# Optimization experiments

Measured on AMD Instinct MI355X. Metric: run time of the kernel, lower is better.

Reference implementation:

```python
import jax, jax.numpy as jnp
import numpy as np

T, D, H = 65536, 256, 256


def setup_inputs() -> dict:
    key = jax.random.key(0)
    ks = jax.random.split(key, 6)
    lim = 1.0 / np.sqrt(H)  # equinox GRUCell init: U(-1/sqrt(hidden), 1/sqrt(hidden))
    x = jax.random.normal(ks[0], (T, D), dtype=jnp.float32)
    state = jnp.zeros((H,), dtype=jnp.float32)
    start = jax.random.randint(ks[1], (T,), 0, 2).astype(jnp.int32)  # episode-start mask
    next_done = jnp.zeros((T,), dtype=jnp.int32)  # unused by forward, kept for signature fidelity
    W_ih = jax.random.uniform(ks[2], (3 * H, D), minval=-lim, maxval=lim, dtype=jnp.float32)
    W_hh = jax.random.uniform(ks[3], (3 * H, H), minval=-lim, maxval=lim, dtype=jnp.float32)
    bias = jax.random.uniform(ks[4], (3 * H,), minval=-lim, maxval=lim, dtype=jnp.float32)
    bias_n = jax.random.uniform(ks[5], (H,), minval=-lim, maxval=lim, dtype=jnp.float32)
    return {"x": x, "state": state, "start": start, "next_done": next_done,
            "W_ih": W_ih, "W_hh": W_hh, "bias": bias, "bias_n": bias_n}


def reference(x, state, start, next_done, W_ih, W_hh, bias, bias_n):
    # Input-dependent gate pre-activations for all timesteps in one big GEMM: [T, 3H]
    igates_all = x @ W_ih.T + bias
    start_f = start.astype(x.dtype)

    def step(h, inp):
        ig, s = inp
        h = h * (1.0 - s)  # reset hidden at episode start (state * logical_not(start))
        hg = W_hh @ h  # [3H]
        r = jax.nn.sigmoid(ig[:H] + hg[:H])
        z = jax.nn.sigmoid(ig[H:2 * H] + hg[H:2 * H])
        n = jnp.tanh(ig[2 * H:] + r * (hg[2 * H:] + bias_n))
        new_h = n + z * (h - n)  # equinox GRUCell output
        return new_h, new_h

    final_state, y = jax.lax.scan(step, state, (igates_all, start_f))
    return y, final_state
```

## Files before the change

kernel.cpp:

```cpp
#include <hip/hip_runtime.h>
#include <hip/hip_bf16.h>
#include <stdint.h>

#define TT   65536
#define NCH  16
#define CNOM 16
#define NBLK 256
#define ROWB 1664

typedef __bf16 bf16x8 __attribute__((ext_vector_type(8)));
typedef float  f32x4  __attribute__((ext_vector_type(4)));
typedef int    i32x4  __attribute__((ext_vector_type(4)));

__device__ __bf16 g_wih[768 * 256];
__device__ __bf16 g_whh[768 * 256];
__device__ __align__(64) unsigned char g_ig[(size_t)TT * ROWB];

__device__ __forceinline__ void gl_lds16(const void* g, void* l) {
  __builtin_amdgcn_global_load_lds(
      (const __attribute__((address_space(1))) void*)(unsigned long long)(uintptr_t)g,
      (__attribute__((address_space(3))) void*)(unsigned int)(uintptr_t)l,
      16, 0, 0);
}

__device__ __forceinline__ float bfbits(uint32_t u) {
  float f; __builtin_memcpy(&f, &u, 4); return f;
}

__device__ __forceinline__ void mfma_bv0(f32x4& acc, bf16x8 a, i32x4 b) {
  asm("v_mfma_f32_16x16x32_bf16 %0, %1, %2, 0" : "=&v"(acc) : "v"(a), "v"(b));
}
__device__ __forceinline__ void mfma_ba0(f32x4& acc, bf16x8 a, i32x4 b) {
  asm("v_mfma_f32_16x16x32_bf16 %0, %1, %2, 0" : "=&v"(acc) : "v"(a), "a"(b));
}
__device__ __forceinline__ void mfma_bv(f32x4& acc, bf16x8 a, i32x4 b) {
  asm("v_mfma_f32_16x16x32_bf16 %0, %1, %2, %0" : "+v"(acc) : "v"(a), "v"(b));
}
__device__ __forceinline__ void mfma_ba(f32x4& acc, bf16x8 a, i32x4 b) {
  asm("v_mfma_f32_16x16x32_bf16 %0, %1, %2, %0" : "+v"(acc) : "v"(a), "a"(b));
}

__global__ void prep_w(const float* __restrict__ wih, const float* __restrict__ whh) {
  const int n = 768 * 256;
  for (int i = blockIdx.x * blockDim.x + threadIdx.x; i < n; i += gridDim.x * blockDim.x) {
    g_wih[i] = (__bf16)wih[i];
    g_whh[i] = (__bf16)whh[i];
  }
}

__global__ __launch_bounds__(256) void gemm_ig(const float* __restrict__ x,
                                               const float* __restrict__ bias) {
  __shared__ __align__(16) __bf16 a_s[128 * 64];
  __shared__ __align__(16) __bf16 b_s[128 * 64];
  const int tid = threadIdx.x;
  const int w = tid >> 6, lane = tid & 63, l15 = lane & 15, q = lane >> 4;
  const int mt = blockIdx.x / 6, ntb = blockIdx.x - mt * 6;
  const int m0 = mt * 128, n0 = ntb * 128;
  const int wm = w >> 1, wn = w & 1;

  f32x4 acc[4][4];
#pragma unroll
  for (int a = 0; a < 4; ++a)
#pragma unroll
    for (int b = 0; b < 4; ++b) acc[a][b] = (f32x4){0.f, 0.f, 0.f, 0.f};

  for (int kc = 0; kc < 4; ++kc) {
#pragma unroll
    for (int i = 0; i < 4; ++i) {
      int pslot = i * 256 + tid;
      int row = pslot >> 3, c = pslot & 7;
      int cs = c ^ (row & 7);
      const float* xs = x + (size_t)(m0 + row) * 256 + kc * 64 + cs * 8;
      float4 f0 = *(const float4*)xs;
      float4 f1 = *(const float4*)(xs + 4);
      bf16x8 v;
      v[0] = (__bf16)f0.x; v[1] = (__bf16)f0.y; v[2] = (__bf16)f0.z; v[3] = (__bf16)f0.w;
      v[4] = (__bf16)f1.x; v[5] = (__bf16)f1.y; v[6] = (__bf16)f1.z; v[7] = (__bf16)f1.w;
      *(bf16x8*)((char*)a_s + pslot * 16) = v;
      gl_lds16((const char*)g_wih + ((size_t)(n0 + row) * 256 + kc * 64) * 2 + cs * 16,
               (char*)b_s + (i * 256 + (tid & ~63)) * 16);
    }
    __syncthreads();
#pragma unroll
    for (int ks = 0; ks < 2; ++ks) {
      bf16x8 af[4], bfr[4];
#pragma unroll
      for (int tm = 0; tm < 4; ++tm) {
        int row = wm * 64 + tm * 16 + l15;
        int cb = (ks * 4 + q) ^ (row & 7);
        af[tm] = *(const bf16x8*)((const char*)a_s + row * 128 + cb * 16);
      }
#pragma unroll
      for (int tn = 0; tn < 4; ++tn) {
        int row = wn * 64 + tn * 16 + l15;
        int cb = (ks * 4 + q) ^ (row & 7);
        bfr[tn] = *(const bf16x8*)((const char*)b_s + row * 128 + cb * 16);
      }
#pragma unroll
      for (int tm = 0; tm < 4; ++tm)
#pragma unroll
        for (int tn = 0; tn < 4; ++tn)
          acc[tm][tn] = __builtin_amdgcn_mfma_f32_16x16x32_bf16(af[tm], bfr[tn], acc[tm][tn], 0, 0, 0);
    }
    __syncthreads();
  }
  float bv[4];
#pragma unroll
  for (int tn = 0; tn < 4; ++tn) bv[tn] = bias[n0 + wn * 64 + tn * 16 + l15];
#pragma unroll
  for (int tm = 0; tm < 4; ++tm) {
#pragma unroll
    for (int tp = 0; tp < 2; ++tp) {
#pragma unroll
      for (int r = 0; r < 4; ++r) {
        int t = m0 + wm * 64 + tm * 16 + q * 4 + r;
        __bf16 lo = (__bf16)(acc[tm][tp * 2][r] + bv[tp * 2]);
        __bf16 hi = (__bf16)(acc[tm][tp * 2 + 1][r] + bv[tp * 2 + 1]);
        unsigned short ulo, uhi;
        __builtin_memcpy(&ulo, &lo, 2); __builtin_memcpy(&uhi, &hi, 2);
        uint32_t u = (uint32_t)ulo | ((uint32_t)uhi << 16);
        *(uint32_t*)(g_ig + (size_t)t * ROWB + ntb * 256 + (wn * 2 + tp) * 64 + l15 * 4) = u;
      }
    }
  }
}

__global__ __launch_bounds__(512)
__attribute__((amdgpu_waves_per_eu(2, 2)))
void gru_scan(const float* __restrict__ state, const int* __restrict__ start,
              const float* __restrict__ bias_n, float* __restrict__ out) {
  __shared__ __align__(16) __bf16 h_s[2][16][264];
  __shared__ __align__(16) unsigned char whh_lds[8 * 16 * 1024];
  __shared__ int flg_s[16 * 132];
  __shared__ int s_arr[17];

  const int tid = threadIdx.x;
  const int w = tid >> 6, lane = tid & 63, l15 = lane & 15, q = lane >> 4;
  const int jrow0 = w * 32 + l15;

  if (tid < 17) {
    int t = (blockIdx.x * NCH + tid) * CNOM;
    if (t > 0) { while (t < TT && start[t] == 0) t++; }
    s_arr[tid] = t;
  }
  for (int i = tid; i < 16 * 264; i += 512) (&h_s[0][0][0])[i] = (__bf16)0.f;
  __syncthreads();

  int sa[4], len[4];
#pragma unroll
  for (int r = 0; r < 4; ++r) {
    sa[r] = s_arr[q * 4 + r];
    len[r] = s_arr[q * 4 + r + 1] - sa[r];
  }
  int ML = 0;
  for (int m = 0; m < 16; ++m) { int L = s_arr[m + 1] - s_arr[m]; ML = L > ML ? L : ML; }
  ML = __builtin_amdgcn_readfirstlane(ML);

  for (int idx = tid; idx < 2048; idx += 512) {
    int m = idx >> 7, kk = idx & 127;
    int t = s_arr[m] + kk;
    flg_s[m * 132 + kk] = (t < TT) ? start[t] : 0;
  }

  char* lp = (char*)whh_lds + w * 16384 + lane * 16;
#pragma unroll
  for (int p = 0; p < 2; ++p)
#pragma unroll
    for (int ks = 0; ks < 8; ++ks) {
      i32x4 t = *(const i32x4*)&g_whh[(size_t)(w * 32 + p * 16 + l15) * 256 + q * 8 + ks * 32];
      *(i32x4*)(lp + (p * 8 + ks) * 1024) = t;
    }
  i32x4 whh_z[2][8], whh_n[2][8];
#pragma unroll
  for (int p = 0; p < 2; ++p)
#pragma unroll
    for (int ks = 0; ks < 8; ++ks) {
      whh_z[p][ks] = *(const i32x4*)&g_whh[(size_t)(1 * 256 + w * 32 + p * 16 + l15) * 256 + q * 8 + ks * 32];
      whh_n[p][ks] = *(const i32x4*)&g_whh[(size_t)(2 * 256 + w * 32 + p * 16 + l15) * 256 + q * 8 + ks * 32];
    }
#pragma unroll
  for (int p = 0; p < 2; ++p)
#pragma unroll
    for (int ks = 0; ks < 8; ++ks) {
      asm volatile("" : "+a"(whh_z[p][ks]));
      asm volatile("" : "+a"(whh_n[p][ks]));
    }

  const float bn2[2] = { bias_n[jrow0], bias_n[jrow0 + 16] };

  const int start0 = start[0];
  if (blockIdx.x == 0 && tid < 256) h_s[0][0][tid] = start0 ? (__bf16)0.f : (__bf16)state[tid];

  float hreg[2][4];
#pragma unroll
  for (int p = 0; p < 2; ++p)
#pragma unroll
    for (int r = 0; r < 4; ++r) hreg[p][r] = 0.f;
  if (blockIdx.x == 0 && q == 0 && !start0) {
    hreg[0][0] = state[jrow0];
    hreg[1][0] = state[jrow0 + 16];
  }

  const int cw = (w >> 2) * 256 + ((w & 3) * 16 + l15) * 4;
  const uint32_t offlim = (uint32_t)(TT - 1) * ROWB + (uint32_t)cw;
  uint32_t off[4];
  float* op[4];
#pragma unroll
  for (int r = 0; r < 4; ++r) {
    off[r] = (uint32_t)sa[r] * ROWB + (uint32_t)cw;
    op[r] = out + (size_t)sa[r] * 256 + jrow0;
  }

  const unsigned char* gig = g_ig;
  uint32_t igA[12], igB[12];
#pragma unroll
  for (int r = 0; r < 4; ++r) {
    igA[r * 3 + 0] = *(const uint32_t*)(gig + off[r]);
    igA[r * 3 + 1] = *(const uint32_t*)(gig + off[r] + 512);
    igA[r * 3 + 2] = *(const uint32_t*)(gig + off[r] + 1024);
    uint32_t nx = off[r] + ROWB; off[r] = nx > offlim ? offlim : nx;
  }
  __syncthreads();

  auto step = [&](int k, uint32_t (&cur)[12], uint32_t (&nxt)[12]) {
#pragma unroll
    for (int r = 0; r < 4; ++r) {
      nxt[r * 3 + 0] = *(const uint32_t*)(gig + off[r]);
      nxt[r * 3 + 1] = *(const uint32_t*)(gig + off[r] + 512);
      nxt[r * 3 + 2] = *(const uint32_t*)(gig + off[r] + 1024);
      uint32_t nx = off[r] + ROWB; off[r] = nx > offlim ? offlim : nx;
    }
    int fnext[4];
    if (k + 1 < 128) {
#pragma unroll
      for (int r = 0; r < 4; ++r) fnext[r] = flg_s[(q * 4 + r) * 132 + k + 1];
    } else {
#pragma unroll
      for (int r = 0; r < 4; ++r) {
        int t = sa[r] + k + 1; t = t > TT - 1 ? TT - 1 : t;
        fnext[r] = start[t];
      }
    }

    const __bf16* hb = &h_s[k & 1][0][0] + l15 * 264 + q * 8;
#pragma unroll
    for (int p = 0; p < 2; ++p) {
      f32x4 a0, a1, a2;
      {
        bf16x8 hf = *(const bf16x8*)(hb);
        i32x4 b0 = *(const i32x4*)(lp + (p * 8) * 1024);
        mfma_bv0(a0, hf, b0);
        mfma_ba0(a1, hf, whh_z[p][0]);
        mfma_ba0(a2, hf, whh_n[p][0]);
      }
#pragma unroll
      for (int ks = 1; ks < 8; ++ks) {
        bf16x8 hf = *(const bf16x8*)(hb + ks * 32);
        i32x4 b0 = *(const i32x4*)(lp + (p * 8 + ks) * 1024);
        mfma_bv(a0, hf, b0);
        mfma_ba(a1, hf, whh_z[p][ks]);
        mfma_ba(a2, hf, whh_n[p][ks]);
      }
      asm volatile("s_nop 7\n\ts_nop 7" : "+v"(a0), "+v"(a1), "+v"(a2));
#pragma unroll
      for (int r = 0; r < 4; ++r) {
        uint32_t vr = cur[r * 3 + 0];
        uint32_t vz = cur[r * 3 + 1];
        uint32_t vn = cur[r * 3 + 2];
        float igr = bfbits(p ? (vr & 0xffff0000u) : (vr << 16));
        float igz = bfbits(p ? (vz & 0xffff0000u) : (vz << 16));
        float ign = bfbits(p ? (vn & 0xffff0000u) : (vn << 16));
        float rp_ = a0[r] + igr;
        float zp_ = a1[r] + igz;
        float hv  = a2[r] + bn2[p];
        float rg = 1.f / (1.f + __expf(-rp_));
        float zg = 1.f / (1.f + __expf(-zp_));
        float np = ign + rg * hv;
        np = fminf(fmaxf(np, -30.f), 30.f);
        float e2 = __expf(2.f * np);
        float ng = (e2 - 1.f) / (e2 + 1.f);
        float hn = ng + zg * (hreg[p][r] - ng);
        if (k < len[r]) op[r][p * 16] = hn;
        hreg[p][r] = fnext[r] ? 0.f : hn;
      }
    }
    __bf16* hw = &h_s[(k + 1) & 1][0][0];
#pragma unroll
    for (int p = 0; p < 2; ++p)
#pragma unroll
      for (int r = 0; r < 4; ++r)
        hw[(q * 4 + r) * 264 + jrow0 + p * 16] = (__bf16)hreg[p][r];
#pragma unroll
    for (int r = 0; r < 4; ++r) op[r] += 256;
    asm volatile("s_waitcnt lgkmcnt(0)" ::: "memory");
    __builtin_amdgcn_s_barrier();
  };

  for (int k = 0; k < ML; ) {
    step(k, igA, igB); ++k;
    if (k < ML) { step(k, igB, igA); ++k; }
  }
}

__global__ void fin_copy(float* __restrict__ out) {
  int i = threadIdx.x;
  out[(size_t)TT * 256 + i] = out[((size_t)TT - 1) * 256 + i];
}

extern "C" void kernel_launch(void* const* d_in, const int* in_sizes, int n_in,
                              void* d_out, int out_size, void* d_ws, size_t ws_size,
                              hipStream_t stream) {
  const float* x      = (const float*)d_in[0];
  const float* state  = (const float*)d_in[1];
  const int*   start  = (const int*)d_in[2];
  const float* wih    = (const float*)d_in[4];
  const float* whh    = (const float*)d_in[5];
  const float* bias   = (const float*)d_in[6];
  const float* bias_n = (const float*)d_in[7];
  float* out = (float*)d_out;

  prep_w<<<256, 256, 0, stream>>>(wih, whh);
  gemm_ig<<<3072, 256, 0, stream>>>(x, bias);
  gru_scan<<<NBLK, 512, 0, stream>>>(state, start, bias_n, out);
  fin_copy<<<1, 256, 0, stream>>>(out);
}
```

Baseline: 304.0 us.

## Keep x tile resident in LDS and stream W_ih with double buffering

The input-gate GEMM now has each 512-thread block own a 128-row strip of x. That strip is converted to bf16 once and kept in LDS across all six 128-column output tiles. W_ih is read as fp32 and converted inline, with double-buffered prefetch of the next chunk, so the separate bf16 copy of W_ih in prep_w goes away. This removes the sixfold re-read and re-conversion of x across blocks. In exchange the grid is smaller (512 blocks), LDS use is larger (96KB), and W_ih is converted redundantly in every block.

```diff
diff --git a/kernel.cpp b/kernel.cpp
--- a/kernel.cpp
+++ b/kernel.cpp
@@ -12,17 +12,9 @@
 typedef float  f32x4  __attribute__((ext_vector_type(4)));
 typedef int    i32x4  __attribute__((ext_vector_type(4)));
 
-__device__ __bf16 g_wih[768 * 256];
 __device__ __bf16 g_whh[768 * 256];
 __device__ __align__(64) unsigned char g_ig[(size_t)TT * ROWB];
 
-__device__ __forceinline__ void gl_lds16(const void* g, void* l) {
-  __builtin_amdgcn_global_load_lds(
-      (const __attribute__((address_space(1))) void*)(unsigned long long)(uintptr_t)g,
-      (__attribute__((address_space(3))) void*)(unsigned int)(uintptr_t)l,
-      16, 0, 0);
-}
-
 __device__ __forceinline__ float bfbits(uint32_t u) {
   float f; __builtin_memcpy(&f, &u, 4); return f;
 }
@@ -40,87 +32,126 @@
   asm("v_mfma_f32_16x16x32_bf16 %0, %1, %2, %0" : "+v"(acc) : "v"(a), "a"(b));
 }
 
-__global__ void prep_w(const float* __restrict__ wih, const float* __restrict__ whh) {
+__device__ __forceinline__ bf16x8 cvt8(float4 f0, float4 f1) {
+  bf16x8 v;
+  v[0] = (__bf16)f0.x; v[1] = (__bf16)f0.y; v[2] = (__bf16)f0.z; v[3] = (__bf16)f0.w;
+  v[4] = (__bf16)f1.x; v[5] = (__bf16)f1.y; v[6] = (__bf16)f1.z; v[7] = (__bf16)f1.w;
+  return v;
+}
+
+__global__ void prep_w(const float* __restrict__ whh) {
   const int n = 768 * 256;
-  for (int i = blockIdx.x * blockDim.x + threadIdx.x; i < n; i += gridDim.x * blockDim.x) {
-    g_wih[i] = (__bf16)wih[i];
+  for (int i = blockIdx.x * blockDim.x + threadIdx.x; i < n; i += gridDim.x * blockDim.x)
     g_whh[i] = (__bf16)whh[i];
-  }
-}
-
-__global__ __launch_bounds__(256) void gemm_ig(const float* __restrict__ x,
+}
+
+__global__ __launch_bounds__(512) void gemm_ig(const float* __restrict__ x,
+                                               const float* __restrict__ wih,
                                                const float* __restrict__ bias) {
-  __shared__ __align__(16) __bf16 a_s[128 * 64];
-  __shared__ __align__(16) __bf16 b_s[128 * 64];
+  __shared__ __align__(16) __bf16 a_s[4][128 * 64];
+  __shared__ __align__(16) __bf16 b_s[2][128 * 64];
   const int tid = threadIdx.x;
-  const int w = tid >> 6, lane = tid & 63, l15 = lane & 15, q = lane >> 4;
-  const int mt = blockIdx.x / 6, ntb = blockIdx.x - mt * 6;
-  const int m0 = mt * 128, n0 = ntb * 128;
-  const int wm = w >> 1, wn = w & 1;
-
-  f32x4 acc[4][4];
-#pragma unroll
-  for (int a = 0; a < 4; ++a)
-#pragma unroll
-    for (int b = 0; b < 4; ++b) acc[a][b] = (f32x4){0.f, 0.f, 0.f, 0.f};
-
-  for (int kc = 0; kc < 4; ++kc) {
-#pragma unroll
-    for (int i = 0; i < 4; ++i) {
-      int pslot = i * 256 + tid;
-      int row = pslot >> 3, c = pslot & 7;
-      int cs = c ^ (row & 7);
+  const int lane = tid & 63, l15 = lane & 15, q = lane >> 4;
+  const int w = tid >> 6;
+  const int wm = w >> 2, wn = w & 3;
+  const int m0 = blockIdx.x * 128;
+
+  float bvA[6], bvB[6];
+#pragma unroll
+  for (int nb = 0; nb < 6; ++nb) {
+    bvA[nb] = bias[nb * 128 + wn * 32 + l15];
+    bvB[nb] = bias[nb * 128 + wn * 32 + 16 + l15];
+  }
+
+#pragma unroll
+  for (int kc = 0; kc < 4; ++kc)
+#pragma unroll
+    for (int i = 0; i < 2; ++i) {
+      int pslot = i * 512 + tid;
+      int row = pslot >> 3, c = pslot & 7, cs = c ^ (row & 7);
       const float* xs = x + (size_t)(m0 + row) * 256 + kc * 64 + cs * 8;
       float4 f0 = *(const float4*)xs;
       float4 f1 = *(const float4*)(xs + 4);
-      bf16x8 v;
-      v[0] = (__bf16)f0.x; v[1] = (__bf16)f0.y; v[2] = (__bf16)f0.z; v[3] = (__bf16)f0.w;
-      v[4] = (__bf16)f1.x; v[5] = (__bf16)f1.y; v[6] = (__bf16)f1.z; v[7] = (__bf16)f1.w;
-      *(bf16x8*)((char*)a_s + pslot * 16) = v;
-      gl_lds16((const char*)g_wih + ((size_t)(n0 + row) * 256 + kc * 64) * 2 + cs * 16,
-               (char*)b_s + (i * 256 + (tid & ~63)) * 16);
-    }
-    __syncthreads();
-#pragma unroll
-    for (int ks = 0; ks < 2; ++ks) {
-      bf16x8 af[4], bfr[4];
-#pragma unroll
-      for (int tm = 0; tm < 4; ++tm) {
-        int row = wm * 64 + tm * 16 + l15;
-        int cb = (ks * 4 + q) ^ (row & 7);
-        af[tm] = *(const bf16x8*)((const char*)a_s + row * 128 + cb * 16);
-      }
-#pragma unroll
-      for (int tn = 0; tn < 4; ++tn) {
-        int row = wn * 64 + tn * 16 + l15;
-        int cb = (ks * 4 + q) ^ (row & 7);
-        bfr[tn] = *(const bf16x8*)((const char*)b_s + row * 128 + cb * 16);
-      }
-#pragma unroll
-      for (int tm = 0; tm < 4; ++tm)
-#pragma unroll
-        for (int tn = 0; tn < 4; ++tn)
-          acc[tm][tn] = __builtin_amdgcn_mfma_f32_16x16x32_bf16(af[tm], bfr[tn], acc[tm][tn], 0, 0, 0);
-    }
-    __syncthreads();
-  }
-  float bv[4];
-#pragma unroll
-  for (int tn = 0; tn < 4; ++tn) bv[tn] = bias[n0 + wn * 64 + tn * 16 + l15];
-#pragma unroll
-  for (int tm = 0; tm < 4; ++tm) {
-#pragma unroll
-    for (int tp = 0; tp < 2; ++tp) {
-#pragma unroll
-      for (int r = 0; r < 4; ++r) {
-        int t = m0 + wm * 64 + tm * 16 + q * 4 + r;
-        __bf16 lo = (__bf16)(acc[tm][tp * 2][r] + bv[tp * 2]);
-        __bf16 hi = (__bf16)(acc[tm][tp * 2 + 1][r] + bv[tp * 2 + 1]);
-        unsigned short ulo, uhi;
-        __builtin_memcpy(&ulo, &lo, 2); __builtin_memcpy(&uhi, &hi, 2);
-        uint32_t u = (uint32_t)ulo | ((uint32_t)uhi << 16);
-        *(uint32_t*)(g_ig + (size_t)t * ROWB + ntb * 256 + (wn * 2 + tp) * 64 + l15 * 4) = u;
-      }
+      *(bf16x8*)((char*)a_s[kc] + pslot * 16) = cvt8(f0, f1);
+    }
+#pragma unroll
+  for (int i = 0; i < 2; ++i) {
+    int pslot = i * 512 + tid;
+    int row = pslot >> 3, c = pslot & 7, cs = c ^ (row & 7);
+    const float* ws = wih + (size_t)(row) * 256 + cs * 8;
+    float4 f0 = *(const float4*)ws;
+    float4 f1 = *(const float4*)(ws + 4);
+    *(bf16x8*)((char*)b_s[0] + pslot * 16) = cvt8(f0, f1);
+  }
+
+  f32x4 acc[4][2];
+#pragma unroll
+  for (int a = 0; a < 4; ++a)
+#pragma unroll
+    for (int b = 0; b < 2; ++b) acc[a][b] = (f32x4){0.f, 0.f, 0.f, 0.f};
+  __syncthreads();
+
+#pragma unroll
+  for (int ntb = 0; ntb < 6; ++ntb) {
+#pragma unroll
+    for (int kc = 0; kc < 4; ++kc) {
+      const int ci = ntb * 4 + kc;
+      const int buf = ci & 1;
+      const int nn = (ci + 1) >> 2, kk = (ci + 1) & 3;
+      const bool more = (ci + 1) < 24;
+      float4 wf00, wf01, wf10, wf11;
+      if (more) {
+        int ps0 = tid, r0 = ps0 >> 3, cs0 = (ps0 & 7) ^ (r0 & 7);
+        const float* ws0 = wih + (size_t)(nn * 128 + r0) * 256 + kk * 64 + cs0 * 8;
+        wf00 = *(const float4*)ws0; wf01 = *(const float4*)(ws0 + 4);
+        int ps1 = 512 + tid, r1 = ps1 >> 3, cs1 = (ps1 & 7) ^ (r1 & 7);
+        const float* ws1 = wih + (size_t)(nn * 128 + r1) * 256 + kk * 64 + cs1 * 8;
+        wf10 = *(const float4*)ws1; wf11 = *(const float4*)(ws1 + 4);
+      }
+#pragma unroll
+      for (int ks = 0; ks < 2; ++ks) {
+        bf16x8 af[4], bfr[2];
+#pragma unroll
+        for (int tm = 0; tm < 4; ++tm) {
+          int row = wm * 64 + tm * 16 + l15;
+          int cb = (ks * 4 + q) ^ (row & 7);
+          af[tm] = *(const bf16x8*)((const char*)a_s[kc] + row * 128 + cb * 16);
+        }
+#pragma unroll
+        for (int tn = 0; tn < 2; ++tn) {
+          int row = wn * 32 + tn * 16 + l15;
+          int cb = (ks * 4 + q) ^ (row & 7);
+          bfr[tn] = *(const bf16x8*)((const char*)b_s[buf] + row * 128 + cb * 16);
+        }
+#pragma unroll
+        for (int tm = 0; tm < 4; ++tm)
+#pragma unroll
+          for (int tn = 0; tn < 2; ++tn)
+            acc[tm][tn] = __builtin_amdgcn_mfma_f32_16x16x32_bf16(af[tm], bfr[tn], acc[tm][tn], 0, 0, 0);
+      }
+      if (more) {
+        *(bf16x8*)((char*)b_s[buf ^ 1] + tid * 16) = cvt8(wf00, wf01);
+        *(bf16x8*)((char*)b_s[buf ^ 1] + (512 + tid) * 16) = cvt8(wf10, wf11);
+      }
+      if (kc == 3) {
+#pragma unroll
+        for (int tm = 0; tm < 4; ++tm)
+#pragma unroll
+          for (int r = 0; r < 4; ++r) {
+            int t = m0 + wm * 64 + tm * 16 + q * 4 + r;
+            __bf16 lo = (__bf16)(acc[tm][0][r] + bvA[ntb]);
+            __bf16 hi = (__bf16)(acc[tm][1][r] + bvB[ntb]);
+            unsigned short ulo, uhi;
+            __builtin_memcpy(&ulo, &lo, 2); __builtin_memcpy(&uhi, &hi, 2);
+            uint32_t u = (uint32_t)ulo | ((uint32_t)uhi << 16);
+            *(uint32_t*)(g_ig + (size_t)t * ROWB + ntb * 256 + wn * 64 + l15 * 4) = u;
+          }
+#pragma unroll
+        for (int a = 0; a < 4; ++a)
+#pragma unroll
+          for (int b = 0; b < 2; ++b) acc[a][b] = (f32x4){0.f, 0.f, 0.f, 0.f};
+      }
+      __syncthreads();
     }
   }
 }
@@ -319,8 +350,8 @@
   const float* bias_n = (const float*)d_in[7];
   float* out = (float*)d_out;
 
-  prep_w<<<256, 256, 0, stream>>>(wih, whh);
-  gemm_ig<<<3072, 256, 0, stream>>>(x, bias);
+  prep_w<<<256, 256, 0, stream>>>(whh);
+  gemm_ig<<<512, 512, 0, stream>>>(x, wih, bias);
   gru_scan<<<NBLK, 512, 0, stream>>>(state, start, bias_n, out);
   fin_copy<<<1, 256, 0, stream>>>(out);
 }
```

New measurement: 281.8 us. 1.08x faster.
